# Kernel tuning notes

Hardware: AMD Instinct MI355X
Metric: run time of the kernel (lower is better)

## Reference

```python
import jax, jax.numpy as jnp
import numpy as np

# Module hyperparameters (from init_kwargs)
H, F = 8, 32            # num_heads, attention_filters
RY, RX = 3, 3           # spatial_radius
PH, PW = 2 * RY + 1, 2 * RX + 1
S = PH * PW             # patch_size = 49
HF = H * F


def setup_inputs() -> dict:
    key = jax.random.key(0)
    ks = jax.random.split(key, 6)
    B, Y, X, C = 4, 64, 64, 256
    x = jax.random.normal(ks[0], (B, Y, X, C), jnp.float32)
    # 1x1 conv kernels == dense matrices over the channel dim (no bias)
    Wq = jax.random.normal(ks[1], (C, HF), jnp.float32) / np.sqrt(C)
    Wk = jax.random.normal(ks[2], (C, HF), jnp.float32) / np.sqrt(C)
    Wv = jax.random.normal(ks[3], (C, HF), jnp.float32) / np.sqrt(C)
    Wo = jax.random.normal(ks[4], (HF, C), jnp.float32) / np.sqrt(HF)
    pos_emb = jax.random.normal(ks[5], (S, HF), jnp.float32) * 0.02
    return {"x": x, "Wq": Wq, "Wk": Wk, "Wv": Wv, "Wo": Wo, "pos_emb": pos_emb}


def reference(x, Wq, Wk, Wv, Wo, pos_emb):
    B, Y, X, C = x.shape
    dtype = x.dtype
    # 1x1 conv projections
    Q = x @ Wq                       # (B,Y,X,HF)
    K = x @ Wk
    V = x @ Wv
    # clipped patch centers (borders reuse interior patches)
    cy = jnp.clip(jnp.arange(Y), RY, Y - RY - 1)   # (Y,)
    cx = jnp.clip(jnp.arange(X), RX, X - RX - 1)   # (X,)
    # query relative-position indices within its patch
    qy = jnp.arange(Y) - cy + RY
    qx = jnp.arange(X) - cx + RX
    qidx = qy[:, None] * PW + qx[None, :]          # (Y,X) in [0,S)
    Q = Q + pos_emb[qidx]                          # add query pos embedding (HF)
    Q = Q.reshape(B, Y, X, H, F)
    K = K.reshape(B, Y, X, H, F)
    V = V.reshape(B, Y, X, H, F)
    cy_g, cx_g = jnp.meshgrid(cy, cx, indexing="ij")  # (Y,X)
    scale = jnp.asarray(1.0 / np.sqrt(F), dtype)
    NEG = jnp.asarray(-1e9, dtype)
    m = jnp.full((B, Y, X, H, 1), NEG, dtype)      # running max
    l = jnp.zeros((B, Y, X, H, 1), dtype)          # running sum-exp
    acc = jnp.zeros((B, Y, X, H, F), dtype)        # running value accumulator
    dy_vec = np.arange(-RY, RY + 1)                # within-chunk offsets ('col' mode)
    for dx in range(-RX, RX + 1):                  # chunk loop over columns (7 chunks)
        ny = jnp.clip(cy_g[None, :, :] + dy_vec[:, None, None], 0, Y - 1)  # (PH,Y,X)
        nx = jnp.clip(cx_g[None, :, :] + dx, 0, X - 1)                     # (1,Y,X)
        nx = jnp.broadcast_to(nx, ny.shape)
        sidx = (dy_vec + RY) * PW + (dx + RX)      # (PH,) relative-pos indices
        # gather neighbor K/V: (B,PH,Y,X,H,F)
        Kc = K[:, ny, nx] + pos_emb[sidx].reshape(PH, 1, 1, H, F)
        Vc = V[:, ny, nx]
        sc = jnp.einsum("byxhf,bsyxhf->byxhs", Q, Kc) * scale  # (B,Y,X,H,PH)
        new_m = jnp.maximum(m, sc.max(axis=-1, keepdims=True))
        alpha = jnp.exp(m - new_m)
        p = jnp.exp(sc - new_m)
        l = l * alpha + p.sum(axis=-1, keepdims=True)
        acc = acc * alpha + jnp.einsum("byxhs,bsyxhf->byxhf", p, Vc)
        m = new_m
    out = (acc / (l + 1e-8)).reshape(B, Y, X, HF) @ Wo
    return out
```

## Files before the change

kernel.cpp:

```cpp
#include <hip/hip_runtime.h>
#include <hip/hip_bf16.h>

static constexpr int NPOS = 4 * 64 * 64;
static constexpr int CD   = 256;
static constexpr int VSTR = 16416;
#define QSCALE (0.17677669529663687f * 1.4426950408889634f)

typedef __attribute__((ext_vector_type(8))) short bf16x8;
typedef __attribute__((ext_vector_type(4))) float f32x4;

__device__ __forceinline__ float bf2f(unsigned short u) {
    return __uint_as_float((unsigned int)u << 16);
}
__device__ __forceinline__ unsigned short bfbits(float f) {
    union { __hip_bfloat16 h; unsigned short u; } cv;
    cv.h = __float2bfloat16(f);
    return cv.u;
}
__device__ __forceinline__ unsigned int packbf2(float lo, float hi) {
    union { __hip_bfloat162 h; unsigned int u; } cv;
    cv.h.x = __float2bfloat16(lo);
    cv.h.y = __float2bfloat16(hi);
    return cv.u;
}
__device__ __forceinline__ uint4 pack8(float4 a, float4 b) {
    uint4 u;
    u.x = packbf2(a.x, a.y); u.y = packbf2(a.z, a.w);
    u.z = packbf2(b.x, b.y); u.w = packbf2(b.z, b.w);
    return u;
}
__device__ __forceinline__ void pl32swap(unsigned &a, unsigned &b) {
    auto r = __builtin_amdgcn_permlane32_swap(a, b, false, false);
    a = r[0]; b = r[1];
}
__device__ __forceinline__ void pl16swap(unsigned &a, unsigned &b) {
    auto r = __builtin_amdgcn_permlane16_swap(a, b, false, false);
    a = r[0]; b = r[1];
}

__global__ __launch_bounds__(256) void convert_kernel(
    const float* __restrict__ Wq, const float* __restrict__ Wk,
    const float* __restrict__ Wv, const float* __restrict__ Wo,
    const float* __restrict__ pe,
    __hip_bfloat16* __restrict__ Wfrag,
    __hip_bfloat16* __restrict__ pebf,
    __hip_bfloat16* __restrict__ Wofrag)
{
    int t = blockIdx.x * 256 + threadIdx.x;
    if (t < 24576) {
        int L = t & 63, ng = (t >> 6) & 7, s = (t >> 9) & 7, T = t >> 12;
        int mat = T >> 1;
        const float* src = (mat == 0) ? Wq : (mat == 1) ? Wk : Wv;
        int ncol  = (T & 1) * 128 + ng * 16 + (L & 15);
        int kbase = s * 32 + (L >> 4) * 8;
        __hip_bfloat16* dst = Wfrag + ((size_t)((T * 8 + s) * 8 + ng) * 64 + L) * 8;
#pragma unroll
        for (int j = 0; j < 8; ++j)
            dst[j] = __float2bfloat16(src[(kbase + j) * 256 + ncol]);
    } else if (t < 26624) {
        int u = t - 24576;
        int L = u & 63, Tn = (u >> 6) & 3, h = u >> 8;
        int s = Tn * 16 + (L & 15);
        int kbase = (L >> 4) * 8;
        __hip_bfloat16* dst = pebf + ((size_t)((h * 4 + Tn) * 64 + L)) * 8;
#pragma unroll
        for (int j = 0; j < 8; ++j) {
            float v = (s < 49) ? pe[s * 256 + h * 32 + kbase + j] * QSCALE : 0.f;
            dst[j] = __float2bfloat16(v);
        }
    } else if (t < 34816) {
        int u = t - 26624;
        int L = u & 63, ng = (u >> 6) & 7, s = (u >> 9) & 7, T = (u >> 12) & 1;
        int ncol  = T * 128 + ng * 16 + (L & 15);
        int kbase = s * 32 + (L >> 4) * 8;
        __hip_bfloat16* dst = Wofrag + ((size_t)((T * 8 + s) * 8 + ng) * 64 + L) * 8;
#pragma unroll
        for (int j = 0; j < 8; ++j)
            dst[j] = __float2bfloat16(Wo[(kbase + j) * 256 + ncol]);
    }
}

__global__ __launch_bounds__(768, 3) void qkv_mfma(
    const float* __restrict__ x,
    const __hip_bfloat16* __restrict__ Wfrag,
    const float* __restrict__ pe,
    unsigned short* __restrict__ QA,
    unsigned short* __restrict__ Kd,
    unsigned short* __restrict__ Vt)
{
    __shared__ __align__(16) unsigned short smem[256 * 68];
    unsigned short* As = smem;
    const int t = threadIdx.x;
    const int rowbase = blockIdx.x * 64;
    const int L = t & 63;
    const int w = t >> 6;
    const int quad = L >> 4, lrow = L & 15;
    const int T = w >> 1;
    const int ngb = (w & 1) * 4;
    const int g = T >> 1;
    const int lw = w & 3;

#pragma unroll
    for (int idx = t; idx < 2048; idx += 768) {
        const int row = idx >> 5, ch8 = idx & 31;
        const float* src = x + (size_t)(rowbase + row) * CD + ch8 * 8;
        float4 f0 = ((const float4*)src)[0];
        float4 f1 = ((const float4*)src)[1];
        *(uint4*)&As[row * 264 + ch8 * 8] = pack8(f0, f1);
    }

    f32x4 acc[4][4];
#pragma unroll
    for (int i = 0; i < 4; ++i)
#pragma unroll
        for (int j = 0; j < 4; ++j) acc[i][j] = (f32x4){0.f, 0.f, 0.f, 0.f};

    const __hip_bfloat16* wbase = Wfrag + ((size_t)(T * 64 + ngb) * 64 + L) * 8;
    bf16x8 bfr[4];
#pragma unroll
    for (int j = 0; j < 4; ++j)
        bfr[j] = *(const bf16x8*)(wbase + (size_t)j * 64 * 8);

    __syncthreads();

#pragma unroll
    for (int s = 0; s < 8; ++s) {
        bf16x8 nbfr[4];
        if (s < 7) {
#pragma unroll
            for (int j = 0; j < 4; ++j)
                nbfr[j] = *(const bf16x8*)(wbase + (size_t)((s + 1) * 8 + j) * 64 * 8);
        }
#pragma unroll
        for (int i = 0; i < 4; ++i) {
            bf16x8 af = *(const bf16x8*)&As[(i * 16 + lrow) * 264 + s * 32 + quad * 8];
#pragma unroll
            for (int j = 0; j < 4; ++j)
                acc[i][j] = __builtin_amdgcn_mfma_f32_16x16x32_bf16(af, bfr[j], acc[i][j], 0, 0, 0);
        }
#pragma unroll
        for (int j = 0; j < 4; ++j) bfr[j] = nbfr[j];
    }

    __syncthreads();

    if (g == 0) {
#pragma unroll
        for (int i = 0; i < 4; ++i)
#pragma unroll
            for (int r = 0; r < 4; ++r) {
                int row = rowbase + i * 16 + quad * 4 + r;
                int yy = (row >> 6) & 63, xx = row & 63;
                int cy = min(max(yy, 3), 60), cx = min(max(xx, 3), 60);
                int qidx = (yy - cy + 3) * 7 + (xx - cx + 3);
#pragma unroll
                for (int j = 0; j < 4; ++j) {
                    int c = lw * 64 + j * 16 + lrow;
                    QA[(size_t)row * CD + c] = bfbits(acc[i][j][r] + pe[qidx * 256 + c]);
                }
            }
    } else if (g == 1) {
#pragma unroll
        for (int i = 0; i < 4; ++i)
#pragma unroll
            for (int r = 0; r < 4; ++r) {
                int row = rowbase + i * 16 + quad * 4 + r;
#pragma unroll
                for (int j = 0; j < 4; ++j) {
                    int c = lw * 64 + j * 16 + lrow;
                    Kd[(size_t)row * CD + c] = bfbits(acc[i][j][r] * QSCALE);
                }
            }
    } else {
        unsigned short* vt = smem;
#pragma unroll
        for (int i = 0; i < 4; ++i)
#pragma unroll
            for (int j = 0; j < 4; ++j) {
                int c = lw * 64 + j * 16 + lrow;
                int row0 = i * 16 + quad * 4;
                *(unsigned int*)&vt[c * 68 + row0] =
                    (unsigned int)bfbits(acc[i][j][0]) | ((unsigned int)bfbits(acc[i][j][1]) << 16);
                *(unsigned int*)&vt[c * 68 + row0 + 2] =
                    (unsigned int)bfbits(acc[i][j][2]) | ((unsigned int)bfbits(acc[i][j][3]) << 16);
            }
    }
    __syncthreads();

    if (g == 2) {
        const int t4 = t - 512;
        const int grp = t4 >> 4, lig = t4 & 15;
        const int row_off = lig * 4;
        unsigned short* vt = smem;
#pragma unroll
        for (int pass = 0; pass < 16; ++pass) {
            int c = pass * 16 + grp;
            *(ushort4*)(Vt + (size_t)c * VSTR + rowbase + row_off) =
                *(const ushort4*)&vt[c * 68 + row_off];
        }
    }
}

__global__ __launch_bounds__(512, 4) void attn_oproj(
    const unsigned short* __restrict__ QA,
    const unsigned short* __restrict__ Kd,
    const unsigned short* __restrict__ Vt,
    const __hip_bfloat16* __restrict__ pebf,
    const __hip_bfloat16* __restrict__ Wofrag,
    float* __restrict__ out)
{
    __shared__ __align__(16) unsigned short qpes[8 * 2 * 1152];
    __shared__ __align__(16) unsigned short At[2 * 16 * 264];
    const int t = threadIdx.x, w = t >> 6, L = t & 63;
    const int lrow = L & 15, quad = L >> 4;
    const int bid = blockIdx.x;
    const int p = ((bid & 7) << 6) | (bid >> 3);
    const int b = p >> 7, ypair = (p >> 2) & 31, x0 = (p & 3) * 16;
    const int yyA = ypair * 2;
    const int pos0a = b * 4096 + yyA * 64 + x0;
    const int pos0b = pos0a + 64;
    const int cyA = min(max(yyA, 3), 60);
    const int cyB = min(max(yyA + 1, 3), 60);
    const int d = cyB - cyA;
    const int nit = 7 + d;
    const int h = w;

    const int kc0 = min(max(x0 - 8 + lrow, 0), 63);
    const int kc1 = min(max(x0 + 8 + lrow, 0), 63);
    const f32x4 zero = {0.f, 0.f, 0.f, 0.f};
    unsigned short* qpA = qpes + w * 2304;
    unsigned short* qpB = qpA + 1152;
    unsigned short* At_a = At;
    unsigned short* At_b = At + 16 * 264;

    const int cx = min(max(x0 + lrow, 3), 60) - x0 + 5;
    int qiA[4], qiB[4];
    float mkA[4], mkB[4];
#pragma unroll
    for (int r = 0; r < 4; ++r) {
        const int sl = quad * 4 + r;
        int dxa = sl - cx;
        qiA[r] = lrow * 72 + min(max(dxa, 0), 6);
        mkA[r] = ((unsigned)dxa <= 6u) ? 1.f : 0.f;
        int dxb = 16 + sl - cx;
        qiB[r] = lrow * 72 + min(max(dxb, 0), 6);
        mkB[r] = ((unsigned)dxb <= 6u) ? 1.f : 0.f;
    }

    const bf16x8 qaA = *(const bf16x8*)(QA + (size_t)(pos0a + lrow) * 256 + h * 32 + quad * 8);
    const bf16x8 qaB = *(const bf16x8*)(QA + (size_t)(pos0b + lrow) * 256 + h * 32 + quad * 8);

#pragma unroll
    for (int Tn = 0; Tn < 4; ++Tn) {
        bf16x8 bp = *(const bf16x8*)(pebf + ((size_t)((h * 4 + Tn) * 64 + L)) * 8);
        f32x4 cA = __builtin_amdgcn_mfma_f32_16x16x32_bf16(bp, qaA, zero, 0, 0, 0);
        f32x4 cB = __builtin_amdgcn_mfma_f32_16x16x32_bf16(bp, qaB, zero, 0, 0, 0);
        *(unsigned int*)&qpA[lrow * 72 + Tn * 16 + quad * 4]     = packbf2(cA[0], cA[1]);
        *(unsigned int*)&qpA[lrow * 72 + Tn * 16 + quad * 4 + 2] = packbf2(cA[2], cA[3]);
        *(unsigned int*)&qpB[lrow * 72 + Tn * 16 + quad * 4]     = packbf2(cB[0], cB[1]);
        *(unsigned int*)&qpB[lrow * 72 + Tn * 16 + quad * 4 + 2] = packbf2(cB[2], cB[3]);
    }
    __builtin_amdgcn_s_waitcnt(0xc07f);

    float laccA = 0.f, laccB = 0.f;
    f32x4 o0a = zero, o1a = zero, o0b = zero, o1b = zero;
    int rowpos = b * 4096 + (cyA - 3) * 64;

    const size_t koff = h * 32 + quad * 8;
    const size_t voff0 = (size_t)(h * 32 + lrow) * VSTR + x0 - 8 + quad * 8;
    const size_t voff1 = (size_t)(h * 32 + 16 + lrow) * VSTR + x0 - 8 + quad * 8;
    bf16x8 bk0 = *(const bf16x8*)(Kd + (size_t)(rowpos + kc0) * 256 + koff);
    bf16x8 bk1 = *(const bf16x8*)(Kd + (size_t)(rowpos + kc1) * 256 + koff);
    bf16x8 bv0 = *(const bf16x8*)(Vt + voff0 + rowpos);
    bf16x8 bv1 = *(const bf16x8*)(Vt + voff1 + rowpos);

    auto tilestep = [&](const bf16x8& qa_, const unsigned short* qp_, int qpofs,
                        float& lacc_, f32x4& o0_, f32x4& o1_) {
        f32x4 s0 = __builtin_amdgcn_mfma_f32_16x16x32_bf16(bk0, qa_, zero, 0, 0, 0);
        f32x4 s1 = __builtin_amdgcn_mfma_f32_16x16x32_bf16(bk1, qa_, zero, 0, 0, 0);
        float e00 = exp2f(s0[0] + bf2f(qp_[qiA[0] + qpofs])) * mkA[0];
        float e01 = exp2f(s0[1] + bf2f(qp_[qiA[1] + qpofs])) * mkA[1];
        float e02 = exp2f(s0[2] + bf2f(qp_[qiA[2] + qpofs])) * mkA[2];
        float e03 = exp2f(s0[3] + bf2f(qp_[qiA[3] + qpofs])) * mkA[3];
        float e10 = exp2f(s1[0] + bf2f(qp_[qiB[0] + qpofs])) * mkB[0];
        float e11 = exp2f(s1[1] + bf2f(qp_[qiB[1] + qpofs])) * mkB[1];
        float e12 = exp2f(s1[2] + bf2f(qp_[qiB[2] + qpofs])) * mkB[2];
        float e13 = exp2f(s1[3] + bf2f(qp_[qiB[3] + qpofs])) * mkB[3];
        lacc_ += ((e00 + e01) + (e02 + e03)) + ((e10 + e11) + (e12 + e13));
        unsigned p0 = packbf2(e00, e01), p1 = packbf2(e02, e03);
        unsigned z0 = packbf2(e10, e11), z1 = packbf2(e12, e13);
        pl32swap(p0, z0); pl16swap(p0, z0);
        pl32swap(p1, z1); pl16swap(p1, z1);
        union { unsigned u[4]; bf16x8 v; } pb;
        pb.u[0] = p0; pb.u[1] = p1; pb.u[2] = z0; pb.u[3] = z1;
        o0_ = __builtin_amdgcn_mfma_f32_16x16x32_bf16(bv0, pb.v, o0_, 0, 0, 0);
        o1_ = __builtin_amdgcn_mfma_f32_16x16x32_bf16(bv1, pb.v, o1_, 0, 0, 0);
    };

    for (int i = 0; i < nit; ++i) {
        const int rnext = rowpos + 64;
        bf16x8 nk0, nk1, nv0, nv1;
        if (i < nit - 1) {
            nk0 = *(const bf16x8*)(Kd + (size_t)(rnext + kc0) * 256 + koff);
            nk1 = *(const bf16x8*)(Kd + (size_t)(rnext + kc1) * 256 + koff);
            nv0 = *(const bf16x8*)(Vt + voff0 + rnext);
            nv1 = *(const bf16x8*)(Vt + voff1 + rnext);
        }
        if (i < 7)
            tilestep(qaA, qpA, i * 7, laccA, o0a, o1a);
        if (i >= d)
            tilestep(qaB, qpB, (i - d) * 7, laccB, o0b, o1b);
        bk0 = nk0; bk1 = nk1; bv0 = nv0; bv1 = nv1;
        rowpos = rnext;
    }

    laccA += __shfl_xor(laccA, 16);
    laccA += __shfl_xor(laccA, 32);
    laccB += __shfl_xor(laccB, 16);
    laccB += __shfl_xor(laccB, 32);
    const float invA = 1.f / (laccA + 1e-8f);
    const float invB = 1.f / (laccB + 1e-8f);
    {
        const int base = lrow * 264 + h * 32 + quad * 4;
        *(unsigned int*)&At_a[base]          = packbf2(o0a[0] * invA, o0a[1] * invA);
        *(unsigned int*)&At_a[base + 2]      = packbf2(o0a[2] * invA, o0a[3] * invA);
        *(unsigned int*)&At_a[base + 16]     = packbf2(o1a[0] * invA, o1a[1] * invA);
        *(unsigned int*)&At_a[base + 16 + 2] = packbf2(o1a[2] * invA, o1a[3] * invA);
        *(unsigned int*)&At_b[base]          = packbf2(o0b[0] * invB, o0b[1] * invB);
        *(unsigned int*)&At_b[base + 2]      = packbf2(o0b[2] * invB, o0b[3] * invB);
        *(unsigned int*)&At_b[base + 16]     = packbf2(o1b[0] * invB, o1b[1] * invB);
        *(unsigned int*)&At_b[base + 16 + 2] = packbf2(o1b[2] * invB, o1b[3] * invB);
    }
    __syncthreads();

    const int T = w >> 2;
    const int ngb = (w & 3) * 2;
    f32x4 accA[2], accB[2];
    accA[0] = zero; accA[1] = zero; accB[0] = zero; accB[1] = zero;

#pragma unroll
    for (int s = 0; s < 8; ++s) {
        bf16x8 bfr[2];
#pragma unroll
        for (int j = 0; j < 2; ++j)
            bfr[j] = *(const bf16x8*)(Wofrag +
                      ((size_t)((T * 8 + s) * 8 + ngb + j) * 64 + L) * 8);
        bf16x8 afA = *(const bf16x8*)(At_a + lrow * 264 + s * 32 + quad * 8);
        bf16x8 afB = *(const bf16x8*)(At_b + lrow * 264 + s * 32 + quad * 8);
#pragma unroll
        for (int j = 0; j < 2; ++j) {
            accA[j] = __builtin_amdgcn_mfma_f32_16x16x32_bf16(afA, bfr[j], accA[j], 0, 0, 0);
            accB[j] = __builtin_amdgcn_mfma_f32_16x16x32_bf16(afB, bfr[j], accB[j], 0, 0, 0);
        }
    }

#pragma unroll
    for (int r = 0; r < 4; ++r) {
        int rowA = pos0a + quad * 4 + r;
        int rowB = pos0b + quad * 4 + r;
#pragma unroll
        for (int j = 0; j < 2; ++j) {
            int c = w * 32 + j * 16 + lrow;
            out[(size_t)rowA * CD + c] = accA[j][r];
            out[(size_t)rowB * CD + c] = accB[j][r];
        }
    }
}

extern "C" void kernel_launch(void* const* d_in, const int* in_sizes, int n_in,
                              void* d_out, int out_size, void* d_ws, size_t ws_size,
                              hipStream_t stream)
{
    const float* x  = (const float*)d_in[0];
    const float* Wq = (const float*)d_in[1];
    const float* Wk = (const float*)d_in[2];
    const float* Wv = (const float*)d_in[3];
    const float* Wo = (const float*)d_in[4];
    const float* pe = (const float*)d_in[5];
    float* out = (float*)d_out;

    char* ws = (char*)d_ws;
    unsigned short* QA = (unsigned short*)ws;
    unsigned short* Kd = (unsigned short*)(ws + (8u << 20));
    unsigned short* Vt = (unsigned short*)(ws + (16u << 20));
    char* fr = ws + (25u << 20) + 4096;
    __hip_bfloat16* Wfrag  = (__hip_bfloat16*)fr;
    __hip_bfloat16* pebf   = (__hip_bfloat16*)(fr + (384u << 10));
    __hip_bfloat16* Wofrag = (__hip_bfloat16*)(fr + (416u << 10));

    convert_kernel<<<136, 256, 0, stream>>>(Wq, Wk, Wv, Wo, pe, Wfrag, pebf, Wofrag);
    qkv_mfma<<<256, 768, 0, stream>>>(x, Wfrag, pe, QA, Kd, Vt);
    attn_oproj<<<512, 512, 0, stream>>>(QA, Kd, Vt, pebf, Wofrag, out);
}
```

Measured before the change: 114.6 us.

## Process four output rows per attention block to reuse K/V loads

Each attention/output-projection block now handles four consecutive image rows instead of two. Every loaded K/V row tile is shared across up to four query rows, and the grid halves to 256 blocks. The Wo fragments are also reused across four rows. This cuts redundant K/V and Wo traffic and loop overhead, but doubles shared memory and register state per block, lowers occupancy (launch bounds 4 to 2), and leaves fewer blocks than a 256-CU part can comfortably balance.

```diff
diff --git a/kernel.cpp b/kernel.cpp
--- a/kernel.cpp
+++ b/kernel.cpp
@@ -201,7 +201,7 @@
     }
 }
 
-__global__ __launch_bounds__(512, 4) void attn_oproj(
+__global__ __launch_bounds__(512, 2) void attn_oproj(
     const unsigned short* __restrict__ QA,
     const unsigned short* __restrict__ Kd,
     const unsigned short* __restrict__ Vt,
@@ -209,29 +209,30 @@
     const __hip_bfloat16* __restrict__ Wofrag,
     float* __restrict__ out)
 {
-    __shared__ __align__(16) unsigned short qpes[8 * 2 * 1152];
-    __shared__ __align__(16) unsigned short At[2 * 16 * 264];
+    __shared__ __align__(16) unsigned short qpes[8 * 4 * 1152];
+    __shared__ __align__(16) unsigned short At[4 * 16 * 264];
     const int t = threadIdx.x, w = t >> 6, L = t & 63;
     const int lrow = L & 15, quad = L >> 4;
     const int bid = blockIdx.x;
-    const int p = ((bid & 7) << 6) | (bid >> 3);
-    const int b = p >> 7, ypair = (p >> 2) & 31, x0 = (p & 3) * 16;
-    const int yyA = ypair * 2;
-    const int pos0a = b * 4096 + yyA * 64 + x0;
-    const int pos0b = pos0a + 64;
+    const int p = ((bid & 7) << 5) | (bid >> 3);
+    const int b = p >> 6, yq = (p >> 2) & 15, x0 = (p & 3) * 16;
+    const int yyA = yq * 4;
+    const int h = w;
     const int cyA = min(max(yyA, 3), 60);
-    const int cyB = min(max(yyA + 1, 3), 60);
-    const int d = cyB - cyA;
-    const int nit = 7 + d;
-    const int h = w;
+    int dd[4], pos0[4];
+#pragma unroll
+    for (int i = 0; i < 4; ++i) {
+        dd[i] = min(max(yyA + i, 3), 60) - cyA;
+        pos0[i] = b * 4096 + (yyA + i) * 64 + x0;
+    }
+    const int nit = 7 + dd[3];
 
     const int kc0 = min(max(x0 - 8 + lrow, 0), 63);
     const int kc1 = min(max(x0 + 8 + lrow, 0), 63);
     const f32x4 zero = {0.f, 0.f, 0.f, 0.f};
-    unsigned short* qpA = qpes + w * 2304;
-    unsigned short* qpB = qpA + 1152;
-    unsigned short* At_a = At;
-    unsigned short* At_b = At + 16 * 264;
+    unsigned short* qp[4];
+#pragma unroll
+    for (int i = 0; i < 4; ++i) qp[i] = qpes + (size_t)(w * 4 + i) * 1152;
 
     const int cx = min(max(x0 + lrow, 3), 60) - x0 + 5;
     int qiA[4], qiB[4];
@@ -247,23 +248,27 @@
         mkB[r] = ((unsigned)dxb <= 6u) ? 1.f : 0.f;
     }
 
-    const bf16x8 qaA = *(const bf16x8*)(QA + (size_t)(pos0a + lrow) * 256 + h * 32 + quad * 8);
-    const bf16x8 qaB = *(const bf16x8*)(QA + (size_t)(pos0b + lrow) * 256 + h * 32 + quad * 8);
+    bf16x8 qa[4];
+#pragma unroll
+    for (int i = 0; i < 4; ++i)
+        qa[i] = *(const bf16x8*)(QA + (size_t)(pos0[i] + lrow) * 256 + h * 32 + quad * 8);
 
 #pragma unroll
     for (int Tn = 0; Tn < 4; ++Tn) {
         bf16x8 bp = *(const bf16x8*)(pebf + ((size_t)((h * 4 + Tn) * 64 + L)) * 8);
-        f32x4 cA = __builtin_amdgcn_mfma_f32_16x16x32_bf16(bp, qaA, zero, 0, 0, 0);
-        f32x4 cB = __builtin_amdgcn_mfma_f32_16x16x32_bf16(bp, qaB, zero, 0, 0, 0);
-        *(unsigned int*)&qpA[lrow * 72 + Tn * 16 + quad * 4]     = packbf2(cA[0], cA[1]);
-        *(unsigned int*)&qpA[lrow * 72 + Tn * 16 + quad * 4 + 2] = packbf2(cA[2], cA[3]);
-        *(unsigned int*)&qpB[lrow * 72 + Tn * 16 + quad * 4]     = packbf2(cB[0], cB[1]);
-        *(unsigned int*)&qpB[lrow * 72 + Tn * 16 + quad * 4 + 2] = packbf2(cB[2], cB[3]);
+#pragma unroll
+        for (int i = 0; i < 4; ++i) {
+            f32x4 c = __builtin_amdgcn_mfma_f32_16x16x32_bf16(bp, qa[i], zero, 0, 0, 0);
+            *(unsigned int*)&qp[i][lrow * 72 + Tn * 16 + quad * 4]     = packbf2(c[0], c[1]);
+            *(unsigned int*)&qp[i][lrow * 72 + Tn * 16 + quad * 4 + 2] = packbf2(c[2], c[3]);
+        }
     }
     __builtin_amdgcn_s_waitcnt(0xc07f);
 
-    float laccA = 0.f, laccB = 0.f;
-    f32x4 o0a = zero, o1a = zero, o0b = zero, o1b = zero;
+    float lacc[4] = {0.f, 0.f, 0.f, 0.f};
+    f32x4 o0[4], o1[4];
+#pragma unroll
+    for (int i = 0; i < 4; ++i) { o0[i] = zero; o1[i] = zero; }
     int rowpos = b * 4096 + (cyA - 3) * 64;
 
     const size_t koff = h * 32 + quad * 8;
@@ -297,46 +302,44 @@
         o1_ = __builtin_amdgcn_mfma_f32_16x16x32_bf16(bv1, pb.v, o1_, 0, 0, 0);
     };
 
-    for (int i = 0; i < nit; ++i) {
+    for (int it = 0; it < nit; ++it) {
         const int rnext = rowpos + 64;
         bf16x8 nk0, nk1, nv0, nv1;
-        if (i < nit - 1) {
+        if (it < nit - 1) {
             nk0 = *(const bf16x8*)(Kd + (size_t)(rnext + kc0) * 256 + koff);
             nk1 = *(const bf16x8*)(Kd + (size_t)(rnext + kc1) * 256 + koff);
             nv0 = *(const bf16x8*)(Vt + voff0 + rnext);
             nv1 = *(const bf16x8*)(Vt + voff1 + rnext);
         }
-        if (i < 7)
-            tilestep(qaA, qpA, i * 7, laccA, o0a, o1a);
-        if (i >= d)
-            tilestep(qaB, qpB, (i - d) * 7, laccB, o0b, o1b);
+#pragma unroll
+        for (int i = 0; i < 4; ++i) {
+            const int dy = it - dd[i];
+            if (dy >= 0 && dy < 7)
+                tilestep(qa[i], qp[i], dy * 7, lacc[i], o0[i], o1[i]);
+        }
         bk0 = nk0; bk1 = nk1; bv0 = nv0; bv1 = nv1;
         rowpos = rnext;
     }
 
-    laccA += __shfl_xor(laccA, 16);
-    laccA += __shfl_xor(laccA, 32);
-    laccB += __shfl_xor(laccB, 16);
-    laccB += __shfl_xor(laccB, 32);
-    const float invA = 1.f / (laccA + 1e-8f);
-    const float invB = 1.f / (laccB + 1e-8f);
-    {
+#pragma unroll
+    for (int i = 0; i < 4; ++i) {
+        lacc[i] += __shfl_xor(lacc[i], 16);
+        lacc[i] += __shfl_xor(lacc[i], 32);
+        const float inv = 1.f / (lacc[i] + 1e-8f);
+        unsigned short* At_i = At + i * 16 * 264;
         const int base = lrow * 264 + h * 32 + quad * 4;
-        *(unsigned int*)&At_a[base]          = packbf2(o0a[0] * invA, o0a[1] * invA);
-        *(unsigned int*)&At_a[base + 2]      = packbf2(o0a[2] * invA, o0a[3] * invA);
-        *(unsigned int*)&At_a[base + 16]     = packbf2(o1a[0] * invA, o1a[1] * invA);
-        *(unsigned int*)&At_a[base + 16 + 2] = packbf2(o1a[2] * invA, o1a[3] * invA);
-        *(unsigned int*)&At_b[base]          = packbf2(o0b[0] * invB, o0b[1] * invB);
-        *(unsigned int*)&At_b[base + 2]      = packbf2(o0b[2] * invB, o0b[3] * invB);
-        *(unsigned int*)&At_b[base + 16]     = packbf2(o1b[0] * invB, o1b[1] * invB);
-        *(unsigned int*)&At_b[base + 16 + 2] = packbf2(o1b[2] * invB, o1b[3] * invB);
+        *(unsigned int*)&At_i[base]          = packbf2(o0[i][0] * inv, o0[i][1] * inv);
+        *(unsigned int*)&At_i[base + 2]      = packbf2(o0[i][2] * inv, o0[i][3] * inv);
+        *(unsigned int*)&At_i[base + 16]     = packbf2(o1[i][0] * inv, o1[i][1] * inv);
+        *(unsigned int*)&At_i[base + 16 + 2] = packbf2(o1[i][2] * inv, o1[i][3] * inv);
     }
     __syncthreads();
 
     const int T = w >> 2;
     const int ngb = (w & 3) * 2;
-    f32x4 accA[2], accB[2];
-    accA[0] = zero; accA[1] = zero; accB[0] = zero; accB[1] = zero;
+    f32x4 acc[4][2];
+#pragma unroll
+    for (int i = 0; i < 4; ++i) { acc[i][0] = zero; acc[i][1] = zero; }
 
 #pragma unroll
     for (int s = 0; s < 8; ++s) {
@@ -345,26 +348,25 @@
         for (int j = 0; j < 2; ++j)
             bfr[j] = *(const bf16x8*)(Wofrag +
                       ((size_t)((T * 8 + s) * 8 + ngb + j) * 64 + L) * 8);
-        bf16x8 afA = *(const bf16x8*)(At_a + lrow * 264 + s * 32 + quad * 8);
-        bf16x8 afB = *(const bf16x8*)(At_b + lrow * 264 + s * 32 + quad * 8);
-#pragma unroll
-        for (int j = 0; j < 2; ++j) {
-            accA[j] = __builtin_amdgcn_mfma_f32_16x16x32_bf16(afA, bfr[j], accA[j], 0, 0, 0);
-            accB[j] = __builtin_amdgcn_mfma_f32_16x16x32_bf16(afB, bfr[j], accB[j], 0, 0, 0);
-        }
-    }
-
-#pragma unroll
-    for (int r = 0; r < 4; ++r) {
-        int rowA = pos0a + quad * 4 + r;
-        int rowB = pos0b + quad * 4 + r;
-#pragma unroll
-        for (int j = 0; j < 2; ++j) {
-            int c = w * 32 + j * 16 + lrow;
-            out[(size_t)rowA * CD + c] = accA[j][r];
-            out[(size_t)rowB * CD + c] = accB[j][r];
-        }
-    }
+#pragma unroll
+        for (int i = 0; i < 4; ++i) {
+            bf16x8 af = *(const bf16x8*)(At + i * 16 * 264 + lrow * 264 + s * 32 + quad * 8);
+            acc[i][0] = __builtin_amdgcn_mfma_f32_16x16x32_bf16(af, bfr[0], acc[i][0], 0, 0, 0);
+            acc[i][1] = __builtin_amdgcn_mfma_f32_16x16x32_bf16(af, bfr[1], acc[i][1], 0, 0, 0);
+        }
+    }
+
+#pragma unroll
+    for (int i = 0; i < 4; ++i)
+#pragma unroll
+        for (int r = 0; r < 4; ++r) {
+            int row = pos0[i] + quad * 4 + r;
+#pragma unroll
+            for (int j = 0; j < 2; ++j) {
+                int c = w * 32 + j * 16 + lrow;
+                out[(size_t)row * CD + c] = acc[i][j][r];
+            }
+        }
 }
 
 extern "C" void kernel_launch(void* const* d_in, const int* in_sizes, int n_in,
@@ -390,5 +392,5 @@
 
     convert_kernel<<<136, 256, 0, stream>>>(Wq, Wk, Wv, Wo, pe, Wfrag, pebf, Wofrag);
     qkv_mfma<<<256, 768, 0, stream>>>(x, Wfrag, pe, QA, Kd, Vt);
-    attn_oproj<<<512, 512, 0, stream>>>(QA, Kd, Vt, pebf, Wofrag, out);
-}
+    attn_oproj<<<256, 512, 0, stream>>>(QA, Kd, Vt, pebf, Wofrag, out);
+}
```

Result: no change. 115.2 us (+0.5%).

## Split attention and output projection; stage K/V rows in shared memory

Applied to the files above, without the earlier changes.

The fused attention+output-projection kernel becomes two kernels. The attention kernel is now indexed by (batch, y-pair, head) and covers a full 64-wide row strip with four waves. It stages each K/V row into double-buffered shared memory, so waves share loads instead of each fetching K/V from global memory. The normalized attention output goes through a global bf16 buffer to a separate output-projection GEMM kernel with 32-row tiles and prefetched Wo fragments. This trades an extra launch and an extra global round trip for better K/V reuse and a larger GEMM tile, plus per-iteration block barriers.

```diff
diff --git a/kernel.cpp b/kernel.cpp
--- a/kernel.cpp
+++ b/kernel.cpp
@@ -201,37 +201,40 @@
     }
 }
 
-__global__ __launch_bounds__(512, 4) void attn_oproj(
+__global__ __launch_bounds__(256, 4) void attn_pass(
     const unsigned short* __restrict__ QA,
     const unsigned short* __restrict__ Kd,
     const unsigned short* __restrict__ Vt,
     const __hip_bfloat16* __restrict__ pebf,
-    const __hip_bfloat16* __restrict__ Wofrag,
-    float* __restrict__ out)
+    unsigned short* __restrict__ Atg)
 {
-    __shared__ __align__(16) unsigned short qpes[8 * 2 * 1152];
-    __shared__ __align__(16) unsigned short At[2 * 16 * 264];
+    __shared__ __align__(16) unsigned short Ks[2][64 * 40];
+    __shared__ __align__(16) unsigned short Vs[2][32 * 88];
+    __shared__ __align__(16) unsigned short qpes[4][2][1152];
     const int t = threadIdx.x, w = t >> 6, L = t & 63;
     const int lrow = L & 15, quad = L >> 4;
     const int bid = blockIdx.x;
-    const int p = ((bid & 7) << 6) | (bid >> 3);
-    const int b = p >> 7, ypair = (p >> 2) & 31, x0 = (p & 3) * 16;
+    const int p = ((bid & 7) << 7) | (bid >> 3);
+    const int ypair = p & 31, h = (p >> 5) & 7, b = p >> 8;
     const int yyA = ypair * 2;
+    const int x0 = w * 16;
     const int pos0a = b * 4096 + yyA * 64 + x0;
     const int pos0b = pos0a + 64;
     const int cyA = min(max(yyA, 3), 60);
-    const int cyB = min(max(yyA + 1, 3), 60);
-    const int d = cyB - cyA;
+    const int d = min(max(yyA + 1, 3), 60) - cyA;
     const int nit = 7 + d;
-    const int h = w;
 
     const int kc0 = min(max(x0 - 8 + lrow, 0), 63);
     const int kc1 = min(max(x0 + 8 + lrow, 0), 63);
     const f32x4 zero = {0.f, 0.f, 0.f, 0.f};
-    unsigned short* qpA = qpes + w * 2304;
-    unsigned short* qpB = qpA + 1152;
-    unsigned short* At_a = At;
-    unsigned short* At_b = At + 16 * 264;
+    unsigned short* qpA = qpes[w][0];
+    unsigned short* qpB = qpes[w][1];
+
+    for (int u = t; u < 512; u += 256) {
+        int bufi = u >> 8, rem = u & 255, ch = rem >> 3, g = rem & 7;
+        int col = (g < 4) ? g * 2 : 72 + (g - 4) * 2;
+        *(unsigned int*)&Vs[bufi][ch * 88 + col] = 0;
+    }
 
     const int cx = min(max(x0 + lrow, 3), 60) - x0 + 5;
     int qiA[4], qiB[4];
@@ -247,6 +250,19 @@
         mkB[r] = ((unsigned)dxb <= 6u) ? 1.f : 0.f;
     }
 
+    auto stage_load = [&](int yrow, uint4& kreg, uint4& vreg) {
+        const int rowg = b * 4096 + yrow * 64;
+        kreg = *(const uint4*)(Kd + (size_t)(rowg + (t >> 2)) * 256 + h * 32 + (t & 3) * 8);
+        vreg = *(const uint4*)(Vt + (size_t)(h * 32 + (t >> 3)) * VSTR + rowg + (t & 7) * 8);
+    };
+    auto stage_write = [&](int bufi, const uint4& kreg, const uint4& vreg) {
+        *(uint4*)&Ks[bufi][(t >> 2) * 40 + (t & 3) * 8] = kreg;
+        *(uint4*)&Vs[bufi][(t >> 3) * 88 + 8 + (t & 7) * 8] = vreg;
+    };
+
+    uint4 kreg, vreg;
+    stage_load(cyA - 3, kreg, vreg);
+
     const bf16x8 qaA = *(const bf16x8*)(QA + (size_t)(pos0a + lrow) * 256 + h * 32 + quad * 8);
     const bf16x8 qaB = *(const bf16x8*)(QA + (size_t)(pos0b + lrow) * 256 + h * 32 + quad * 8);
 
@@ -260,58 +276,51 @@
         *(unsigned int*)&qpB[lrow * 72 + Tn * 16 + quad * 4]     = packbf2(cB[0], cB[1]);
         *(unsigned int*)&qpB[lrow * 72 + Tn * 16 + quad * 4 + 2] = packbf2(cB[2], cB[3]);
     }
-    __builtin_amdgcn_s_waitcnt(0xc07f);
+    stage_write(0, kreg, vreg);
+    __syncthreads();
 
     float laccA = 0.f, laccB = 0.f;
     f32x4 o0a = zero, o1a = zero, o0b = zero, o1b = zero;
-    int rowpos = b * 4096 + (cyA - 3) * 64;
-
-    const size_t koff = h * 32 + quad * 8;
-    const size_t voff0 = (size_t)(h * 32 + lrow) * VSTR + x0 - 8 + quad * 8;
-    const size_t voff1 = (size_t)(h * 32 + 16 + lrow) * VSTR + x0 - 8 + quad * 8;
-    bf16x8 bk0 = *(const bf16x8*)(Kd + (size_t)(rowpos + kc0) * 256 + koff);
-    bf16x8 bk1 = *(const bf16x8*)(Kd + (size_t)(rowpos + kc1) * 256 + koff);
-    bf16x8 bv0 = *(const bf16x8*)(Vt + voff0 + rowpos);
-    bf16x8 bv1 = *(const bf16x8*)(Vt + voff1 + rowpos);
-
-    auto tilestep = [&](const bf16x8& qa_, const unsigned short* qp_, int qpofs,
-                        float& lacc_, f32x4& o0_, f32x4& o1_) {
-        f32x4 s0 = __builtin_amdgcn_mfma_f32_16x16x32_bf16(bk0, qa_, zero, 0, 0, 0);
-        f32x4 s1 = __builtin_amdgcn_mfma_f32_16x16x32_bf16(bk1, qa_, zero, 0, 0, 0);
-        float e00 = exp2f(s0[0] + bf2f(qp_[qiA[0] + qpofs])) * mkA[0];
-        float e01 = exp2f(s0[1] + bf2f(qp_[qiA[1] + qpofs])) * mkA[1];
-        float e02 = exp2f(s0[2] + bf2f(qp_[qiA[2] + qpofs])) * mkA[2];
-        float e03 = exp2f(s0[3] + bf2f(qp_[qiA[3] + qpofs])) * mkA[3];
-        float e10 = exp2f(s1[0] + bf2f(qp_[qiB[0] + qpofs])) * mkB[0];
-        float e11 = exp2f(s1[1] + bf2f(qp_[qiB[1] + qpofs])) * mkB[1];
-        float e12 = exp2f(s1[2] + bf2f(qp_[qiB[2] + qpofs])) * mkB[2];
-        float e13 = exp2f(s1[3] + bf2f(qp_[qiB[3] + qpofs])) * mkB[3];
-        lacc_ += ((e00 + e01) + (e02 + e03)) + ((e10 + e11) + (e12 + e13));
-        unsigned p0 = packbf2(e00, e01), p1 = packbf2(e02, e03);
-        unsigned z0 = packbf2(e10, e11), z1 = packbf2(e12, e13);
-        pl32swap(p0, z0); pl16swap(p0, z0);
-        pl32swap(p1, z1); pl16swap(p1, z1);
-        union { unsigned u[4]; bf16x8 v; } pb;
-        pb.u[0] = p0; pb.u[1] = p1; pb.u[2] = z0; pb.u[3] = z1;
-        o0_ = __builtin_amdgcn_mfma_f32_16x16x32_bf16(bv0, pb.v, o0_, 0, 0, 0);
-        o1_ = __builtin_amdgcn_mfma_f32_16x16x32_bf16(bv1, pb.v, o1_, 0, 0, 0);
-    };
-
-    for (int i = 0; i < nit; ++i) {
-        const int rnext = rowpos + 64;
-        bf16x8 nk0, nk1, nv0, nv1;
-        if (i < nit - 1) {
-            nk0 = *(const bf16x8*)(Kd + (size_t)(rnext + kc0) * 256 + koff);
-            nk1 = *(const bf16x8*)(Kd + (size_t)(rnext + kc1) * 256 + koff);
-            nv0 = *(const bf16x8*)(Vt + voff0 + rnext);
-            nv1 = *(const bf16x8*)(Vt + voff1 + rnext);
-        }
-        if (i < 7)
-            tilestep(qaA, qpA, i * 7, laccA, o0a, o1a);
-        if (i >= d)
-            tilestep(qaB, qpB, (i - d) * 7, laccB, o0b, o1b);
-        bk0 = nk0; bk1 = nk1; bv0 = nv0; bv1 = nv1;
-        rowpos = rnext;
+    int buf = 0;
+
+    for (int it = 0; it < nit; ++it) {
+        const bool pf = (it + 1 < nit);
+        if (pf) stage_load(cyA - 3 + it + 1, kreg, vreg);
+
+        bf16x8 bk0 = *(const bf16x8*)&Ks[buf][kc0 * 40 + quad * 8];
+        bf16x8 bk1 = *(const bf16x8*)&Ks[buf][kc1 * 40 + quad * 8];
+        bf16x8 bv0 = *(const bf16x8*)&Vs[buf][lrow * 88 + x0 + quad * 8];
+        bf16x8 bv1 = *(const bf16x8*)&Vs[buf][(16 + lrow) * 88 + x0 + quad * 8];
+
+        auto tilestep = [&](const bf16x8& qa_, const unsigned short* qp_, int qpofs,
+                            float& lacc_, f32x4& o0_, f32x4& o1_) {
+            f32x4 s0 = __builtin_amdgcn_mfma_f32_16x16x32_bf16(bk0, qa_, zero, 0, 0, 0);
+            f32x4 s1 = __builtin_amdgcn_mfma_f32_16x16x32_bf16(bk1, qa_, zero, 0, 0, 0);
+            float e00 = exp2f(s0[0] + bf2f(qp_[qiA[0] + qpofs])) * mkA[0];
+            float e01 = exp2f(s0[1] + bf2f(qp_[qiA[1] + qpofs])) * mkA[1];
+            float e02 = exp2f(s0[2] + bf2f(qp_[qiA[2] + qpofs])) * mkA[2];
+            float e03 = exp2f(s0[3] + bf2f(qp_[qiA[3] + qpofs])) * mkA[3];
+            float e10 = exp2f(s1[0] + bf2f(qp_[qiB[0] + qpofs])) * mkB[0];
+            float e11 = exp2f(s1[1] + bf2f(qp_[qiB[1] + qpofs])) * mkB[1];
+            float e12 = exp2f(s1[2] + bf2f(qp_[qiB[2] + qpofs])) * mkB[2];
+            float e13 = exp2f(s1[3] + bf2f(qp_[qiB[3] + qpofs])) * mkB[3];
+            lacc_ += ((e00 + e01) + (e02 + e03)) + ((e10 + e11) + (e12 + e13));
+            unsigned p0 = packbf2(e00, e01), p1 = packbf2(e02, e03);
+            unsigned z0 = packbf2(e10, e11), z1 = packbf2(e12, e13);
+            pl32swap(p0, z0); pl16swap(p0, z0);
+            pl32swap(p1, z1); pl16swap(p1, z1);
+            union { unsigned u[4]; bf16x8 v; } pb;
+            pb.u[0] = p0; pb.u[1] = p1; pb.u[2] = z0; pb.u[3] = z1;
+            o0_ = __builtin_amdgcn_mfma_f32_16x16x32_bf16(bv0, pb.v, o0_, 0, 0, 0);
+            o1_ = __builtin_amdgcn_mfma_f32_16x16x32_bf16(bv1, pb.v, o1_, 0, 0, 0);
+        };
+
+        if (it < 7)  tilestep(qaA, qpA, it * 7, laccA, o0a, o1a);
+        if (it >= d) tilestep(qaB, qpB, (it - d) * 7, laccB, o0b, o1b);
+
+        if (pf) stage_write(buf ^ 1, kreg, vreg);
+        __syncthreads();
+        buf ^= 1;
     }
 
     laccA += __shfl_xor(laccA, 16);
@@ -321,50 +330,83 @@
     const float invA = 1.f / (laccA + 1e-8f);
     const float invB = 1.f / (laccB + 1e-8f);
     {
-        const int base = lrow * 264 + h * 32 + quad * 4;
-        *(unsigned int*)&At_a[base]          = packbf2(o0a[0] * invA, o0a[1] * invA);
-        *(unsigned int*)&At_a[base + 2]      = packbf2(o0a[2] * invA, o0a[3] * invA);
-        *(unsigned int*)&At_a[base + 16]     = packbf2(o1a[0] * invA, o1a[1] * invA);
-        *(unsigned int*)&At_a[base + 16 + 2] = packbf2(o1a[2] * invA, o1a[3] * invA);
-        *(unsigned int*)&At_b[base]          = packbf2(o0b[0] * invB, o0b[1] * invB);
-        *(unsigned int*)&At_b[base + 2]      = packbf2(o0b[2] * invB, o0b[3] * invB);
-        *(unsigned int*)&At_b[base + 16]     = packbf2(o1b[0] * invB, o1b[1] * invB);
-        *(unsigned int*)&At_b[base + 16 + 2] = packbf2(o1b[2] * invB, o1b[3] * invB);
-    }
+        const int baseA = (pos0a + lrow) * 256 + h * 32 + quad * 4;
+        *(unsigned int*)&Atg[baseA]      = packbf2(o0a[0] * invA, o0a[1] * invA);
+        *(unsigned int*)&Atg[baseA + 2]  = packbf2(o0a[2] * invA, o0a[3] * invA);
+        *(unsigned int*)&Atg[baseA + 16] = packbf2(o1a[0] * invA, o1a[1] * invA);
+        *(unsigned int*)&Atg[baseA + 18] = packbf2(o1a[2] * invA, o1a[3] * invA);
+        const int baseB = (pos0b + lrow) * 256 + h * 32 + quad * 4;
+        *(unsigned int*)&Atg[baseB]      = packbf2(o0b[0] * invB, o0b[1] * invB);
+        *(unsigned int*)&Atg[baseB + 2]  = packbf2(o0b[2] * invB, o0b[3] * invB);
+        *(unsigned int*)&Atg[baseB + 16] = packbf2(o1b[0] * invB, o1b[1] * invB);
+        *(unsigned int*)&Atg[baseB + 18] = packbf2(o1b[2] * invB, o1b[3] * invB);
+    }
+}
+
+__global__ __launch_bounds__(256, 4) void oproj(
+    const unsigned short* __restrict__ Atg,
+    const __hip_bfloat16* __restrict__ Wofrag,
+    float* __restrict__ out)
+{
+    __shared__ __align__(16) unsigned short As2[32 * 264];
+    const int t = threadIdx.x, w = t >> 6, L = t & 63;
+    const int lrow = L & 15, quad = L >> 4;
+    const int rowbase = blockIdx.x * 32;
+
+#pragma unroll
+    for (int k = 0; k < 4; ++k) {
+        int idx = t + k * 256;
+        int row = idx >> 5, ch8 = idx & 31;
+        *(uint4*)&As2[row * 264 + ch8 * 8] =
+            *(const uint4*)(Atg + (size_t)(rowbase + row) * 256 + ch8 * 8);
+    }
+
+    const int T = w >> 1;
+    const int ngb = (w & 1) * 4;
+    f32x4 acc[2][4];
+#pragma unroll
+    for (int i = 0; i < 2; ++i)
+#pragma unroll
+        for (int j = 0; j < 4; ++j) acc[i][j] = (f32x4){0.f, 0.f, 0.f, 0.f};
+
+    const __hip_bfloat16* wbase = Wofrag + ((size_t)(T * 64 + ngb) * 64 + L) * 8;
+    bf16x8 bfr[4];
+#pragma unroll
+    for (int j = 0; j < 4; ++j)
+        bfr[j] = *(const bf16x8*)(wbase + (size_t)j * 64 * 8);
+
     __syncthreads();
 
-    const int T = w >> 2;
-    const int ngb = (w & 3) * 2;
-    f32x4 accA[2], accB[2];
-    accA[0] = zero; accA[1] = zero; accB[0] = zero; accB[1] = zero;
-
 #pragma unroll
     for (int s = 0; s < 8; ++s) {
-        bf16x8 bfr[2];
-#pragma unroll
-        for (int j = 0; j < 2; ++j)
-            bfr[j] = *(const bf16x8*)(Wofrag +
-                      ((size_t)((T * 8 + s) * 8 + ngb + j) * 64 + L) * 8);
-        bf16x8 afA = *(const bf16x8*)(At_a + lrow * 264 + s * 32 + quad * 8);
-        bf16x8 afB = *(const bf16x8*)(At_b + lrow * 264 + s * 32 + quad * 8);
-#pragma unroll
-        for (int j = 0; j < 2; ++j) {
-            accA[j] = __builtin_amdgcn_mfma_f32_16x16x32_bf16(afA, bfr[j], accA[j], 0, 0, 0);
-            accB[j] = __builtin_amdgcn_mfma_f32_16x16x32_bf16(afB, bfr[j], accB[j], 0, 0, 0);
-        }
-    }
-
-#pragma unroll
-    for (int r = 0; r < 4; ++r) {
-        int rowA = pos0a + quad * 4 + r;
-        int rowB = pos0b + quad * 4 + r;
-#pragma unroll
-        for (int j = 0; j < 2; ++j) {
-            int c = w * 32 + j * 16 + lrow;
-            out[(size_t)rowA * CD + c] = accA[j][r];
-            out[(size_t)rowB * CD + c] = accB[j][r];
-        }
-    }
+        bf16x8 nbfr[4];
+        if (s < 7) {
+#pragma unroll
+            for (int j = 0; j < 4; ++j)
+                nbfr[j] = *(const bf16x8*)(wbase + (size_t)((s + 1) * 8 + j) * 64 * 8);
+        }
+#pragma unroll
+        for (int i = 0; i < 2; ++i) {
+            bf16x8 af = *(const bf16x8*)&As2[(i * 16 + lrow) * 264 + s * 32 + quad * 8];
+#pragma unroll
+            for (int j = 0; j < 4; ++j)
+                acc[i][j] = __builtin_amdgcn_mfma_f32_16x16x32_bf16(af, bfr[j], acc[i][j], 0, 0, 0);
+        }
+#pragma unroll
+        for (int j = 0; j < 4; ++j) bfr[j] = nbfr[j];
+    }
+
+#pragma unroll
+    for (int i = 0; i < 2; ++i)
+#pragma unroll
+        for (int r = 0; r < 4; ++r) {
+            int row = rowbase + i * 16 + quad * 4 + r;
+#pragma unroll
+            for (int j = 0; j < 4; ++j) {
+                int c = w * 64 + j * 16 + lrow;
+                out[(size_t)row * CD + c] = acc[i][j][r];
+            }
+        }
 }
 
 extern "C" void kernel_launch(void* const* d_in, const int* in_sizes, int n_in,
@@ -380,15 +422,17 @@
     float* out = (float*)d_out;
 
     char* ws = (char*)d_ws;
-    unsigned short* QA = (unsigned short*)ws;
-    unsigned short* Kd = (unsigned short*)(ws + (8u << 20));
-    unsigned short* Vt = (unsigned short*)(ws + (16u << 20));
+    unsigned short* QA  = (unsigned short*)ws;
+    unsigned short* Kd  = (unsigned short*)(ws + (8u << 20));
+    unsigned short* Vt  = (unsigned short*)(ws + (16u << 20));
     char* fr = ws + (25u << 20) + 4096;
     __hip_bfloat16* Wfrag  = (__hip_bfloat16*)fr;
     __hip_bfloat16* pebf   = (__hip_bfloat16*)(fr + (384u << 10));
     __hip_bfloat16* Wofrag = (__hip_bfloat16*)(fr + (416u << 10));
+    unsigned short* Atg = (unsigned short*)(ws + (32u << 20));
 
     convert_kernel<<<136, 256, 0, stream>>>(Wq, Wk, Wv, Wo, pe, Wfrag, pebf, Wofrag);
     qkv_mfma<<<256, 768, 0, stream>>>(x, Wfrag, pe, QA, Kd, Vt);
-    attn_oproj<<<512, 512, 0, stream>>>(QA, Kd, Vt, pebf, Wofrag, out);
-}
+    attn_pass<<<1024, 256, 0, stream>>>(QA, Kd, Vt, pebf, Atg);
+    oproj<<<512, 256, 0, stream>>>(Atg, Wofrag, out);
+}
```

New measurement: 118.4 us. 3.3% more time.
